# Kernel tuning notes

Hardware: AMD Instinct MI355X
Metric: run time of the kernel (lower is better)

## Reference

```python
import jax, jax.numpy as jnp
import numpy as np

N_NODES = 50000
N_EDGES = 600000
IN_F = 128
OUT_F = 128
SMALL = max(IN_F // 10, 1)  # floor(128/10) = 12
D_K = np.sqrt(SMALL).astype(np.float32)


def setup_inputs() -> dict:
    key = jax.random.key(0)
    ks = jax.random.split(key, 10)
    node_data = jax.random.normal(ks[0], (N_NODES, IN_F), dtype=jnp.float32)
    src = jax.random.randint(ks[1], (N_EDGES,), 0, N_NODES, dtype=jnp.int32)
    dst = jax.random.randint(ks[2], (N_EDGES,), 0, N_NODES, dtype=jnp.int32)
    s_q = 1.0 / np.sqrt(IN_F)
    Wq = jax.random.uniform(ks[3], (SMALL, IN_F), jnp.float32, -s_q, s_q)
    bq = jax.random.uniform(ks[4], (SMALL,), jnp.float32, -s_q, s_q)
    Wk = jax.random.uniform(ks[5], (SMALL, IN_F), jnp.float32, -s_q, s_q)
    bk = jax.random.uniform(ks[6], (SMALL,), jnp.float32, -s_q, s_q)
    W1 = jax.random.uniform(ks[7], (OUT_F, IN_F), jnp.float32, -s_q, s_q)
    W2 = jax.random.uniform(ks[8], (OUT_F, IN_F), jnp.float32, -s_q, s_q)
    b2 = jax.random.uniform(ks[9], (OUT_F,), jnp.float32, -s_q, s_q)
    return {"node_data": node_data, "src": src, "dst": dst,
            "Wq": Wq, "bq": bq, "Wk": Wk, "bk": bk,
            "W1": W1, "W2": W2, "b2": b2}


def reference(node_data, src, dst, Wq, bq, Wk, bk, W1, W2, b2):
    N = node_data.shape[0]
    # dgl.add_self_loop: append (i, i) for every node -> each dst has >= 1 edge
    loops = jnp.arange(N, dtype=src.dtype)
    s = jnp.concatenate([src, loops])
    d = jnp.concatenate([dst, loops])

    # query = Tanh(Linear), key = Linear  (shapes [N, SMALL])
    q = jnp.tanh(node_data @ Wq.T + bq)
    k = node_data @ Wk.T + bk

    # per-edge score: sum(query[src] * key[dst]) / sqrt(small)
    scores = jnp.sum(q[s] * k[d], axis=1) / D_K  # [E]

    # softmax over incoming edges of each dst node (segment softmax)
    seg_max = jax.ops.segment_max(scores, d, num_segments=N)
    w = jnp.exp(scores - seg_max[d])
    seg_sum = jax.ops.segment_sum(w, d, num_segments=N)
    w = w / seg_sum[d]  # [E]

    # weighted scatter-aggregate of src node inputs -> [N, IN_F]
    att = jax.ops.segment_sum(w[:, None] * node_data[s], d, num_segments=N)

    # DeepSetLayer: layer1(node_data) + layer2(node attention)
    x = node_data @ W1.T + (att @ W2.T + b2)
    # per-row L2 ('fro' over dim=1) normalization, then ReLU
    x = x / jnp.linalg.norm(x, axis=1, keepdims=True)
    return jax.nn.relu(x)
```

## Files before the change

kernel.cpp:

```cpp
#include <hip/hip_runtime.h>
#include <hip/hip_bf16.h>
#include <math.h>
#include <stdint.h>


#define IN_F 128
#define SMALL 12
#define QK_PAD 16

#define SCAN_ITEMS 8
#define SCAN_CHUNK 2048

typedef __attribute__((ext_vector_type(8))) short short8;
typedef __attribute__((ext_vector_type(4))) float f32x4;

__device__ __forceinline__ unsigned short f2bf(float f) {
    union { float f; unsigned u; } v; v.f = f;
    unsigned r = v.u + 0x7fff + ((v.u >> 16) & 1);
    return (unsigned short)(r >> 16);
}

__device__ __forceinline__ float2 bf2x2(unsigned v) {
    union { unsigned u; float f; } a, b;
    a.u = v << 16;
    b.u = v & 0xffff0000u;
    return make_float2(a.f, b.f);
}

__device__ __forceinline__ float dot12(const float* __restrict__ qrow,
                                       float4 k0, float4 k1, float4 k2) {
    float4 a = ((const float4*)qrow)[0];
    float4 b = ((const float4*)qrow)[1];
    float4 c = ((const float4*)qrow)[2];
    return a.x*k0.x + a.y*k0.y + a.z*k0.z + a.w*k0.w
         + b.x*k1.x + b.y*k1.y + b.z*k1.z + b.w*k1.w
         + c.x*k2.x + c.y*k2.y + c.z*k2.z + c.w*k2.w;
}

__device__ __forceinline__ short8 ld_bf8(const float* p) {
    float4 x0 = *(const float4*)p;
    float4 x1 = *(const float4*)(p + 4);
    short8 a;
    a[0] = (short)f2bf(x0.x); a[1] = (short)f2bf(x0.y);
    a[2] = (short)f2bf(x0.z); a[3] = (short)f2bf(x0.w);
    a[4] = (short)f2bf(x1.x); a[5] = (short)f2bf(x1.y);
    a[6] = (short)f2bf(x1.z); a[7] = (short)f2bf(x1.w);
    return a;
}

__global__ __launch_bounds__(256) void prep_kernel(
    const float* __restrict__ nd,
    const float* __restrict__ Wq, const float* __restrict__ bq,
    const float* __restrict__ Wk, const float* __restrict__ bk,
    const int* __restrict__ dst,
    const float* __restrict__ W1, const float* __restrict__ W2,
    float* __restrict__ q, float* __restrict__ kf,
    unsigned short* __restrict__ ndb, int* __restrict__ cnt,
    unsigned short* __restrict__ rank, unsigned short* __restrict__ Wc,
    int N, int E, int NBQK, int NBCNT)
{
    int t = threadIdx.x;
    int b = blockIdx.x;

    if (b < NBQK) {
        int wv = t >> 6;
        int lane = t & 63;
        int col = lane & 15;
        int quad = lane >> 4;
        int tbase = b * 64 + wv * 16;

        int arow = tbase + col;
        int rowc = (arow < N) ? arow : (N - 1);
        const float* ap = nd + (size_t)rowc * IN_F + quad * 8;
        unsigned short* np = ndb + (size_t)arow * IN_F + quad * 8;

        const float* w0 = ((col < 12) ? (Wq + (size_t)col * IN_F)
                                      : (Wk + (size_t)(col - 12) * IN_F)) + quad * 8;
        const float* w1 = Wk + (size_t)((col < 8) ? (col + 4) : 4) * IN_F + quad * 8;
        bool hasw1 = (col < 8);

        f32x4 acc0 = (f32x4)0.f, acc1 = (f32x4)0.f;
#pragma unroll
        for (int ks = 0; ks < 4; ks++) {
            int k0 = ks * 32;
            short8 a = ld_bf8(ap + k0);
            if (arow < N) *(short8*)(np + k0) = a;
            short8 b0 = ld_bf8(w0 + k0);
            short8 b1 = hasw1 ? ld_bf8(w1 + k0) : (short8)0;
            acc0 = __builtin_amdgcn_mfma_f32_16x16x32_bf16(a, b0, acc0, 0, 0, 0);
            acc1 = __builtin_amdgcn_mfma_f32_16x16x32_bf16(a, b1, acc1, 0, 0, 0);
        }

        float bias0 = (col < 12) ? bq[col] : bk[col - 12];
        float bias1 = (col < 8) ? bk[col + 4] : 0.f;
#pragma unroll
        for (int r = 0; r < 4; r++) {
            int node = tbase + quad * 4 + r;
            if (node < N) {
                float v0 = acc0[r] + bias0;
                if (col < 12) {
                    q[(size_t)node * QK_PAD + col] = tanhf(v0);
                } else {
                    kf[(size_t)node * QK_PAD + (col - 12)] = v0;
                }
                if (hasw1)
                    kf[(size_t)node * QK_PAD + col + 4] = acc1[r] + bias1;
            }
        }
    } else if (b < NBQK + NBCNT) {
        int ET = E + N;
        int stride = NBCNT * 256;
        for (int i = (b - NBQK) * 256 + t; i < ET; i += stride) {
            int d = (i < E) ? dst[i] : (i - E);
            rank[i] = (unsigned short)atomicAdd(&cnt[d], 1);
        }
    } else {
        int idx = (b - NBQK - NBCNT) * 256 + t;
        int f = idx >> 8, k = idx & 255;
        float v = (k < 128) ? W1[f * 128 + k] : W2[f * 128 + (k - 128)];
        Wc[idx] = f2bf(v);
    }
}

__global__ __launch_bounds__(256) void scan_local_kernel(
    int* __restrict__ off, int* __restrict__ bsum, int N)
{
    __shared__ int tsum[256];
    int t = threadIdx.x;
    int base = blockIdx.x * SCAN_CHUNK + t * SCAN_ITEMS;
    int v[SCAN_ITEMS];
    int s = 0;
#pragma unroll
    for (int i = 0; i < SCAN_ITEMS; i++) {
        int idx = base + i;
        v[i] = (idx < N) ? off[idx] : 0;
        s += v[i];
    }
    tsum[t] = s;
    __syncthreads();
    for (int d = 1; d < 256; d <<= 1) {
        int x = (t >= d) ? tsum[t - d] : 0;
        __syncthreads();
        tsum[t] += x;
        __syncthreads();
    }
    int excl = (t == 0) ? 0 : tsum[t - 1];
#pragma unroll
    for (int i = 0; i < SCAN_ITEMS; i++) {
        int idx = base + i;
        if (idx < N) off[idx] = excl;
        excl += v[i];
    }
    if (t == 255) bsum[blockIdx.x] = tsum[255];
}

__global__ __launch_bounds__(256) void scan_add_kernel(
    int* __restrict__ off, const int* __restrict__ bsum, int N, int NB)
{
    __shared__ int pre2[2];
    int t = threadIdx.x;
    if (t == 0) {
        int p = 0, tot = 0;
        for (int i = 0; i < NB; i++) {
            int v = bsum[i];
            if (i < (int)blockIdx.x) p += v;
            tot += v;
        }
        pre2[0] = p; pre2[1] = tot;
    }
    __syncthreads();
    int add = pre2[0];
    if (blockIdx.x == 0 && t == 0) off[N] = pre2[1];

    int base = blockIdx.x * SCAN_CHUNK + t * SCAN_ITEMS;
#pragma unroll
    for (int i = 0; i < SCAN_ITEMS; i++) {
        int j = base + i;
        if (j < N) off[j] += add;
    }
}

__global__ __launch_bounds__(256) void scatter_kernel(
    const int* __restrict__ src, const int* __restrict__ dst,
    const int* __restrict__ off, const unsigned short* __restrict__ rank,
    unsigned short* __restrict__ esrc, int E, int N)
{
    int i = blockIdx.x * 256 + threadIdx.x;
    if (i >= E + N) return;
    int d, s;
    if (i < E) { d = dst[i]; s = src[i]; }
    else       { d = i - E; s = d; }
    esrc[off[d] + (int)rank[i]] = (unsigned short)s;
}

__global__ __launch_bounds__(256) void attn_kernel(
    const unsigned short* __restrict__ ndb, const float* __restrict__ q,
    const float* __restrict__ kf, const int* __restrict__ off,
    const unsigned short* __restrict__ esrc, float* __restrict__ att, int N)
{
    const float INVDK = 0.28867513459481287f;
    int wid = blockIdx.x * 4 + (threadIdx.x >> 6);
    if (wid >= N) return;
    int lane = threadIdx.x & 63;

    int start = off[wid];
    int deg = off[wid + 1] - start;

    const float4* kp = (const float4*)(kf + (size_t)wid * QK_PAD);
    float4 k0 = kp[0], k1 = kp[1], k2 = kp[2];

    float2 acc = make_float2(0.f, 0.f);
    float inv;

    if (deg <= 64) {
        float sc = -INFINITY;
        int si = 0;
        if (lane < deg) {
            si = (int)esrc[start + lane];
            sc = dot12(q + (size_t)si * QK_PAD, k0, k1, k2) * INVDK;
        }
        float m = sc;
#pragma unroll
        for (int o = 32; o > 0; o >>= 1) m = fmaxf(m, __shfl_xor(m, o));
        float w = (lane < deg) ? __expf(sc - m) : 0.f;
        float lsum = w;
#pragma unroll
        for (int o = 32; o > 0; o >>= 1) lsum += __shfl_xor(lsum, o);
        inv = 1.f / lsum;

        unsigned cur[16], nxt[16];
#pragma unroll
        for (int u = 0; u < 16; u++) {
            int r = __shfl(si, u);
            if (u < deg)
                cur[u] = *(const unsigned*)(ndb + (size_t)r * IN_F + lane * 2);
        }
        for (int b0 = 0; b0 < deg; b0 += 16) {
#pragma unroll
            for (int u = 0; u < 16; u++) {
                int idx = b0 + 16 + u;
                int r = __shfl(si, idx & 63);
                if (idx < deg)
                    nxt[u] = *(const unsigned*)(ndb + (size_t)r * IN_F + lane * 2);
            }
#pragma unroll
            for (int u = 0; u < 16; u++) {
                int idx = b0 + u;
                if (idx < deg) {
                    float wi = __shfl(w, idx);
                    float2 f = bf2x2(cur[u]);
                    acc.x += wi * f.x;
                    acc.y += wi * f.y;
                }
            }
#pragma unroll
            for (int u = 0; u < 16; u++) cur[u] = nxt[u];
        }
    } else {
        float m = -INFINITY;
        for (int i = lane; i < deg; i += 64) {
            int s2 = (int)esrc[start + i];
            m = fmaxf(m, dot12(q + (size_t)s2 * QK_PAD, k0, k1, k2) * INVDK);
        }
#pragma unroll
        for (int o = 32; o > 0; o >>= 1) m = fmaxf(m, __shfl_xor(m, o));
        float lsum = 0.f;
        for (int i = lane; i < deg; i += 64) {
            int s2 = (int)esrc[start + i];
            lsum += __expf(dot12(q + (size_t)s2 * QK_PAD, k0, k1, k2) * INVDK - m);
        }
#pragma unroll
        for (int o = 32; o > 0; o >>= 1) lsum += __shfl_xor(lsum, o);
        inv = 1.f / lsum;
        for (int base = 0; base < deg; base += 64) {
            int cnt2 = deg - base; if (cnt2 > 64) cnt2 = 64;
            float w = 0.f; int si = 0;
            if (lane < cnt2) {
                si = (int)esrc[start + base + lane];
                w = __expf(dot12(q + (size_t)si * QK_PAD, k0, k1, k2) * INVDK - m);
            }
            for (int i = 0; i < cnt2; i++) {
                float wi = __shfl(w, i);
                int r = __shfl(si, i);
                float2 f = bf2x2(*(const unsigned*)(ndb + (size_t)r * IN_F + lane * 2));
                acc.x += wi * f.x;
                acc.y += wi * f.y;
            }
        }
    }
    acc.x *= inv; acc.y *= inv;
    ((float2*)(att + (size_t)wid * IN_F))[lane] = acc;
}

__global__ __launch_bounds__(256) void final_kernel(
    const unsigned short* __restrict__ ndb, const float* __restrict__ nd,
    const float* __restrict__ att,
    const unsigned short* __restrict__ Wc, const float* __restrict__ b2,
    float* __restrict__ out, int N)
{
    int wv = threadIdx.x >> 6;
    int lane = threadIdx.x & 63;
    int col = lane & 15;
    int quad = lane >> 4;

    int arow = blockIdx.x * 64 + wv * 16 + col;
    int rowc = (arow < N) ? arow : (N - 1);
    const unsigned short* a0p = ndb + (size_t)rowc * IN_F + quad * 8;
    const float* a1p = ((arow < N) ? att : nd) + (size_t)rowc * IN_F + quad * 8;

    f32x4 acc[8];
#pragma unroll
    for (int i = 0; i < 8; i++) acc[i] = (f32x4)0.f;

#pragma unroll
    for (int ks = 0; ks < 8; ks++) {
        int k0 = ks * 32;
        short8 a;
        if (ks < 4) {
            a = *(const short8*)(a0p + k0);
        } else {
            a = ld_bf8(a1p + (k0 - 128));
        }
#pragma unroll
        for (int ft = 0; ft < 8; ft++) {
            int n = ft * 16 + col;
            short8 b = *(const short8*)(Wc + (size_t)n * 256 + k0 + quad * 8);
            acc[ft] = __builtin_amdgcn_mfma_f32_16x16x32_bf16(a, b, acc[ft], 0, 0, 0);
        }
    }

    float bias[8];
#pragma unroll
    for (int ft = 0; ft < 8; ft++) bias[ft] = b2[ft * 16 + col];

#pragma unroll
    for (int r = 0; r < 4; r++) {
        int node = blockIdx.x * 64 + wv * 16 + quad * 4 + r;
        float v[8];
        float ps = 0.f;
#pragma unroll
        for (int ft = 0; ft < 8; ft++) {
            v[ft] = acc[ft][r] + bias[ft];
            ps += v[ft] * v[ft];
        }
        ps += __shfl_xor(ps, 1);
        ps += __shfl_xor(ps, 2);
        ps += __shfl_xor(ps, 4);
        ps += __shfl_xor(ps, 8);
        float rn = rsqrtf(ps);
        if (node < N) {
            float* op = out + (size_t)node * 128 + col;
#pragma unroll
            for (int ft = 0; ft < 8; ft++)
                op[ft * 16] = fmaxf(v[ft] * rn, 0.f);
        }
    }
}

static inline char* align_up(char* p, size_t a) {
    return (char*)(((uintptr_t)p + (a - 1)) & ~(uintptr_t)(a - 1));
}

extern "C" void kernel_launch(void* const* d_in, const int* in_sizes, int n_in,
                              void* d_out, int out_size, void* d_ws, size_t ws_size,
                              hipStream_t stream) {
    const float* node_data = (const float*)d_in[0];
    const int*   src       = (const int*)d_in[1];
    const int*   dst       = (const int*)d_in[2];
    const float* Wq        = (const float*)d_in[3];
    const float* bq        = (const float*)d_in[4];
    const float* Wk        = (const float*)d_in[5];
    const float* bk        = (const float*)d_in[6];
    const float* W1        = (const float*)d_in[7];
    const float* W2        = (const float*)d_in[8];
    const float* b2        = (const float*)d_in[9];
    float* out = (float*)d_out;

    int N = in_sizes[0] / IN_F;
    int E = in_sizes[1];
    int ET = E + N;
    int NB = (N + SCAN_CHUNK - 1) / SCAN_CHUNK;
    int NBQK = (N + 63) / 64;
    int NBCNT = 512;
    int NBCVT = 128;

    char* w = (char*)d_ws;
    float* q  = (float*)w;  w += (size_t)N * QK_PAD * sizeof(float);
    float* kf = (float*)w;  w += (size_t)N * QK_PAD * sizeof(float);
    w = align_up(w, 256);
    unsigned short* ndb = (unsigned short*)w;  w += (size_t)N * IN_F * sizeof(unsigned short);
    w = align_up(w, 256);
    unsigned short* Wc = (unsigned short*)w;  w += 128 * 256 * sizeof(unsigned short);
    int* off    = (int*)w;  w += (size_t)(N + 1) * sizeof(int);
    int* bsum   = (int*)w;  w += 256 * sizeof(int);
    unsigned short* rank = (unsigned short*)w;  w += (size_t)ET * sizeof(unsigned short);
    w = align_up(w, 256);
    unsigned short* esrc = (unsigned short*)w;  w += (size_t)ET * sizeof(unsigned short);
    float* att = out;

    hipMemsetAsync(off, 0, (size_t)(N + 1) * sizeof(int), stream);

    prep_kernel<<<NBQK + NBCNT + NBCVT, 256, 0, stream>>>(
        node_data, Wq, bq, Wk, bk, dst, W1, W2,
        q, kf, ndb, off, rank, Wc, N, E, NBQK, NBCNT);
    scan_local_kernel<<<NB, 256, 0, stream>>>(off, bsum, N);
    scan_add_kernel<<<NB, 256, 0, stream>>>(off, bsum, N, NB);
    scatter_kernel<<<(ET + 255) / 256, 256, 0, stream>>>(src, dst, off, rank, esrc, E, N);
    attn_kernel<<<(N + 3) / 4, 256, 0, stream>>>(ndb, q, kf, off, esrc, att, N);
    final_kernel<<<(N + 63) / 64, 256, 0, stream>>>(ndb, node_data, att, Wc, b2, out, N);
}
```

Measured before the change: 226.6 us.

## Fuse all stages into one persistent cooperative kernel with grid syncs

Replaces the memset plus six separate kernel launches with a single cooperative persistent kernel that loops over work with grid-stride loops and separates the stages with grid.sync(). It also simplifies the attention gather loop from a 16-deep double-buffered prefetch to a 4-way unrolled loop. The intent is to remove launch overhead and inter-kernel gaps. In exchange it limits parallelism to one resident grid of at most 1024 blocks, pays for six grid-wide barriers, and hides less gather latency.

```diff
diff --git a/kernel.cpp b/kernel.cpp
--- a/kernel.cpp
+++ b/kernel.cpp
@@ -1,13 +1,15 @@
 #include <hip/hip_runtime.h>
+#include <hip/hip_cooperative_groups.h>
 #include <hip/hip_bf16.h>
 #include <math.h>
 #include <stdint.h>
 
+namespace cg = cooperative_groups;
+
 
 #define IN_F 128
 #define SMALL 12
 #define QK_PAD 16
-
 #define SCAN_ITEMS 8
 #define SCAN_CHUNK 2048
 
@@ -28,13 +30,13 @@
 }
 
 __device__ __forceinline__ float dot12(const float* __restrict__ qrow,
-                                       float4 k0, float4 k1, float4 k2) {
+                                       float4 c0, float4 c1, float4 c2) {
     float4 a = ((const float4*)qrow)[0];
     float4 b = ((const float4*)qrow)[1];
     float4 c = ((const float4*)qrow)[2];
-    return a.x*k0.x + a.y*k0.y + a.z*k0.z + a.w*k0.w
-         + b.x*k1.x + b.y*k1.y + b.z*k1.z + b.w*k1.w
-         + c.x*k2.x + c.y*k2.y + c.z*k2.z + c.w*k2.w;
+    return a.x*c0.x + a.y*c0.y + a.z*c0.z + a.w*c0.w
+         + b.x*c1.x + b.y*c1.y + b.z*c1.z + b.w*c1.w
+         + c.x*c2.x + c.y*c2.y + c.z*c2.z + c.w*c2.w;
 }
 
 __device__ __forceinline__ short8 ld_bf8(const float* p) {
@@ -48,27 +50,40 @@
     return a;
 }
 
-__global__ __launch_bounds__(256) void prep_kernel(
-    const float* __restrict__ nd,
+__global__ __launch_bounds__(256, 4) void mega_kernel(
+    const float* __restrict__ nd, const int* __restrict__ src,
+    const int* __restrict__ dst,
     const float* __restrict__ Wq, const float* __restrict__ bq,
     const float* __restrict__ Wk, const float* __restrict__ bk,
-    const int* __restrict__ dst,
     const float* __restrict__ W1, const float* __restrict__ W2,
+    const float* __restrict__ b2,
     float* __restrict__ q, float* __restrict__ kf,
-    unsigned short* __restrict__ ndb, int* __restrict__ cnt,
-    unsigned short* __restrict__ rank, unsigned short* __restrict__ Wc,
-    int N, int E, int NBQK, int NBCNT)
+    unsigned short* __restrict__ ndb, unsigned short* __restrict__ Wc,
+    int* __restrict__ off, int* __restrict__ bsum,
+    unsigned short* __restrict__ rank, unsigned short* __restrict__ esrc,
+    float* __restrict__ out, int N, int E)
 {
+    cg::grid_group grid = cg::this_grid();
+    __shared__ int tsum[256];
+    __shared__ int pre2[2];
+
     int t = threadIdx.x;
     int b = blockIdx.x;
-
-    if (b < NBQK) {
-        int wv = t >> 6;
-        int lane = t & 63;
-        int col = lane & 15;
-        int quad = lane >> 4;
-        int tbase = b * 64 + wv * 16;
-
+    int NBLK = gridDim.x;
+    int gsz = NBLK * 256;
+    int gid = b * 256 + t;
+    int ET = E + N;
+    int wv = t >> 6;
+    int lane = t & 63;
+    int col = lane & 15;
+    int quad = lane >> 4;
+    int NT = (N + 63) >> 6;
+
+    for (int i = gid; i <= N; i += gsz) off[i] = 0;
+    grid.sync();
+
+    for (int tb = b; tb < NT; tb += NBLK) {
+        int tbase = tb * 64 + wv * 16;
         int arow = tbase + col;
         int rowc = (arow < N) ? arow : (N - 1);
         const float* ap = nd + (size_t)rowc * IN_F + quad * 8;
@@ -85,12 +100,11 @@
             int k0 = ks * 32;
             short8 a = ld_bf8(ap + k0);
             if (arow < N) *(short8*)(np + k0) = a;
-            short8 b0 = ld_bf8(w0 + k0);
-            short8 b1 = hasw1 ? ld_bf8(w1 + k0) : (short8)0;
-            acc0 = __builtin_amdgcn_mfma_f32_16x16x32_bf16(a, b0, acc0, 0, 0, 0);
-            acc1 = __builtin_amdgcn_mfma_f32_16x16x32_bf16(a, b1, acc1, 0, 0, 0);
-        }
-
+            short8 bb0 = ld_bf8(w0 + k0);
+            short8 bb1 = hasw1 ? ld_bf8(w1 + k0) : (short8)0;
+            acc0 = __builtin_amdgcn_mfma_f32_16x16x32_bf16(a, bb0, acc0, 0, 0, 0);
+            acc1 = __builtin_amdgcn_mfma_f32_16x16x32_bf16(a, bb1, acc1, 0, 0, 0);
+        }
         float bias0 = (col < 12) ? bq[col] : bk[col - 12];
         float bias1 = (col < 8) ? bk[col + 4] : 0.f;
 #pragma unroll
@@ -98,261 +112,224 @@
             int node = tbase + quad * 4 + r;
             if (node < N) {
                 float v0 = acc0[r] + bias0;
-                if (col < 12) {
-                    q[(size_t)node * QK_PAD + col] = tanhf(v0);
-                } else {
-                    kf[(size_t)node * QK_PAD + (col - 12)] = v0;
-                }
-                if (hasw1)
-                    kf[(size_t)node * QK_PAD + col + 4] = acc1[r] + bias1;
-            }
-        }
-    } else if (b < NBQK + NBCNT) {
-        int ET = E + N;
-        int stride = NBCNT * 256;
-        for (int i = (b - NBQK) * 256 + t; i < ET; i += stride) {
-            int d = (i < E) ? dst[i] : (i - E);
-            rank[i] = (unsigned short)atomicAdd(&cnt[d], 1);
-        }
-    } else {
-        int idx = (b - NBQK - NBCNT) * 256 + t;
-        int f = idx >> 8, k = idx & 255;
+                if (col < 12) q[(size_t)node * QK_PAD + col] = tanhf(v0);
+                else          kf[(size_t)node * QK_PAD + (col - 12)] = v0;
+                if (hasw1)    kf[(size_t)node * QK_PAD + col + 4] = acc1[r] + bias1;
+            }
+        }
+    }
+    for (int i = gid; i < ET; i += gsz) {
+        int d = (i < E) ? dst[i] : (i - E);
+        rank[i] = (unsigned short)atomicAdd(&off[d], 1);
+    }
+    for (int i = gid; i < 128 * 256; i += gsz) {
+        int f = i >> 8, k = i & 255;
         float v = (k < 128) ? W1[f * 128 + k] : W2[f * 128 + (k - 128)];
-        Wc[idx] = f2bf(v);
-    }
-}
-
-__global__ __launch_bounds__(256) void scan_local_kernel(
-    int* __restrict__ off, int* __restrict__ bsum, int N)
-{
-    __shared__ int tsum[256];
-    int t = threadIdx.x;
-    int base = blockIdx.x * SCAN_CHUNK + t * SCAN_ITEMS;
-    int v[SCAN_ITEMS];
-    int s = 0;
-#pragma unroll
-    for (int i = 0; i < SCAN_ITEMS; i++) {
-        int idx = base + i;
-        v[i] = (idx < N) ? off[idx] : 0;
-        s += v[i];
-    }
-    tsum[t] = s;
-    __syncthreads();
-    for (int d = 1; d < 256; d <<= 1) {
-        int x = (t >= d) ? tsum[t - d] : 0;
+        Wc[i] = f2bf(v);
+    }
+    grid.sync();
+
+    int NBS = (N + SCAN_CHUNK - 1) / SCAN_CHUNK;
+    if (b < NBS) {
+        int base = b * SCAN_CHUNK + t * SCAN_ITEMS;
+        int v[SCAN_ITEMS];
+        int s = 0;
+#pragma unroll
+        for (int i = 0; i < SCAN_ITEMS; i++) {
+            int idx = base + i;
+            v[i] = (idx < N) ? off[idx] : 0;
+            s += v[i];
+        }
+        tsum[t] = s;
         __syncthreads();
-        tsum[t] += x;
+        for (int d = 1; d < 256; d <<= 1) {
+            int x = (t >= d) ? tsum[t - d] : 0;
+            __syncthreads();
+            tsum[t] += x;
+            __syncthreads();
+        }
+        int excl = (t == 0) ? 0 : tsum[t - 1];
+#pragma unroll
+        for (int i = 0; i < SCAN_ITEMS; i++) {
+            int idx = base + i;
+            if (idx < N) off[idx] = excl;
+            excl += v[i];
+        }
+        if (t == 255) bsum[b] = tsum[255];
+    }
+    grid.sync();
+
+    if (b < NBS) {
+        if (t == 0) {
+            int p = 0, tot = 0;
+            for (int i = 0; i < NBS; i++) {
+                int v = bsum[i];
+                if (i < b) p += v;
+                tot += v;
+            }
+            pre2[0] = p; pre2[1] = tot;
+        }
         __syncthreads();
-    }
-    int excl = (t == 0) ? 0 : tsum[t - 1];
-#pragma unroll
-    for (int i = 0; i < SCAN_ITEMS; i++) {
-        int idx = base + i;
-        if (idx < N) off[idx] = excl;
-        excl += v[i];
-    }
-    if (t == 255) bsum[blockIdx.x] = tsum[255];
-}
-
-__global__ __launch_bounds__(256) void scan_add_kernel(
-    int* __restrict__ off, const int* __restrict__ bsum, int N, int NB)
-{
-    __shared__ int pre2[2];
-    int t = threadIdx.x;
-    if (t == 0) {
-        int p = 0, tot = 0;
-        for (int i = 0; i < NB; i++) {
-            int v = bsum[i];
-            if (i < (int)blockIdx.x) p += v;
-            tot += v;
-        }
-        pre2[0] = p; pre2[1] = tot;
-    }
-    __syncthreads();
-    int add = pre2[0];
-    if (blockIdx.x == 0 && t == 0) off[N] = pre2[1];
-
-    int base = blockIdx.x * SCAN_CHUNK + t * SCAN_ITEMS;
-#pragma unroll
-    for (int i = 0; i < SCAN_ITEMS; i++) {
-        int j = base + i;
-        if (j < N) off[j] += add;
-    }
-}
-
-__global__ __launch_bounds__(256) void scatter_kernel(
-    const int* __restrict__ src, const int* __restrict__ dst,
-    const int* __restrict__ off, const unsigned short* __restrict__ rank,
-    unsigned short* __restrict__ esrc, int E, int N)
-{
-    int i = blockIdx.x * 256 + threadIdx.x;
-    if (i >= E + N) return;
-    int d, s;
-    if (i < E) { d = dst[i]; s = src[i]; }
-    else       { d = i - E; s = d; }
-    esrc[off[d] + (int)rank[i]] = (unsigned short)s;
-}
-
-__global__ __launch_bounds__(256) void attn_kernel(
-    const unsigned short* __restrict__ ndb, const float* __restrict__ q,
-    const float* __restrict__ kf, const int* __restrict__ off,
-    const unsigned short* __restrict__ esrc, float* __restrict__ att, int N)
-{
-    const float INVDK = 0.28867513459481287f;
-    int wid = blockIdx.x * 4 + (threadIdx.x >> 6);
-    if (wid >= N) return;
-    int lane = threadIdx.x & 63;
-
-    int start = off[wid];
-    int deg = off[wid + 1] - start;
-
-    const float4* kp = (const float4*)(kf + (size_t)wid * QK_PAD);
-    float4 k0 = kp[0], k1 = kp[1], k2 = kp[2];
-
-    float2 acc = make_float2(0.f, 0.f);
-    float inv;
-
-    if (deg <= 64) {
-        float sc = -INFINITY;
-        int si = 0;
-        if (lane < deg) {
-            si = (int)esrc[start + lane];
-            sc = dot12(q + (size_t)si * QK_PAD, k0, k1, k2) * INVDK;
-        }
-        float m = sc;
-#pragma unroll
-        for (int o = 32; o > 0; o >>= 1) m = fmaxf(m, __shfl_xor(m, o));
-        float w = (lane < deg) ? __expf(sc - m) : 0.f;
-        float lsum = w;
-#pragma unroll
-        for (int o = 32; o > 0; o >>= 1) lsum += __shfl_xor(lsum, o);
-        inv = 1.f / lsum;
-
-        unsigned cur[16], nxt[16];
-#pragma unroll
-        for (int u = 0; u < 16; u++) {
-            int r = __shfl(si, u);
-            if (u < deg)
-                cur[u] = *(const unsigned*)(ndb + (size_t)r * IN_F + lane * 2);
-        }
-        for (int b0 = 0; b0 < deg; b0 += 16) {
-#pragma unroll
-            for (int u = 0; u < 16; u++) {
-                int idx = b0 + 16 + u;
-                int r = __shfl(si, idx & 63);
-                if (idx < deg)
-                    nxt[u] = *(const unsigned*)(ndb + (size_t)r * IN_F + lane * 2);
-            }
-#pragma unroll
-            for (int u = 0; u < 16; u++) {
-                int idx = b0 + u;
-                if (idx < deg) {
-                    float wi = __shfl(w, idx);
-                    float2 f = bf2x2(cur[u]);
+        int add = pre2[0];
+        if (b == 0 && t == 0) off[N] = pre2[1];
+        int base = b * SCAN_CHUNK + t * SCAN_ITEMS;
+#pragma unroll
+        for (int i = 0; i < SCAN_ITEMS; i++) {
+            int j = base + i;
+            if (j < N) off[j] += add;
+        }
+    }
+    grid.sync();
+
+    for (int i = gid; i < ET; i += gsz) {
+        int d, s;
+        if (i < E) { d = dst[i]; s = src[i]; }
+        else       { d = i - E; s = d; }
+        esrc[off[d] + (int)rank[i]] = (unsigned short)s;
+    }
+    grid.sync();
+
+    {
+        const float INVDK = 0.28867513459481287f;
+        float* att = out;
+        for (int wid = b * 4 + wv; wid < N; wid += NBLK * 4) {
+            int start = off[wid];
+            int deg = off[wid + 1] - start;
+
+            const float4* kp = (const float4*)(kf + (size_t)wid * QK_PAD);
+            float4 c0 = kp[0], c1 = kp[1], c2 = kp[2];
+
+            float2 acc = make_float2(0.f, 0.f);
+            float inv;
+
+            if (deg <= 64) {
+                float sc = -INFINITY;
+                int si = 0;
+                if (lane < deg) {
+                    si = (int)esrc[start + lane];
+                    sc = dot12(q + (size_t)si * QK_PAD, c0, c1, c2) * INVDK;
+                }
+                float m = sc;
+#pragma unroll
+                for (int o = 32; o > 0; o >>= 1) m = fmaxf(m, __shfl_xor(m, o));
+                float w = (lane < deg) ? __expf(sc - m) : 0.f;
+                float lsum = w;
+#pragma unroll
+                for (int o = 32; o > 0; o >>= 1) lsum += __shfl_xor(lsum, o);
+                inv = 1.f / lsum;
+
+                int i = 0;
+                for (; i + 4 <= deg; i += 4) {
+                    float w0 = __shfl(w, i);     int r0 = __shfl(si, i);
+                    float w1 = __shfl(w, i + 1); int r1 = __shfl(si, i + 1);
+                    float w2 = __shfl(w, i + 2); int r2 = __shfl(si, i + 2);
+                    float w3 = __shfl(w, i + 3); int r3 = __shfl(si, i + 3);
+                    unsigned v0 = *(const unsigned*)(ndb + (size_t)r0 * IN_F + lane * 2);
+                    unsigned v1 = *(const unsigned*)(ndb + (size_t)r1 * IN_F + lane * 2);
+                    unsigned v2 = *(const unsigned*)(ndb + (size_t)r2 * IN_F + lane * 2);
+                    unsigned v3 = *(const unsigned*)(ndb + (size_t)r3 * IN_F + lane * 2);
+                    float2 f0 = bf2x2(v0), f1 = bf2x2(v1), f2 = bf2x2(v2), f3 = bf2x2(v3);
+                    acc.x += w0 * f0.x + w1 * f1.x + w2 * f2.x + w3 * f3.x;
+                    acc.y += w0 * f0.y + w1 * f1.y + w2 * f2.y + w3 * f3.y;
+                }
+                for (; i < deg; i++) {
+                    float wi = __shfl(w, i);
+                    int r = __shfl(si, i);
+                    float2 f = bf2x2(*(const unsigned*)(ndb + (size_t)r * IN_F + lane * 2));
                     acc.x += wi * f.x;
                     acc.y += wi * f.y;
                 }
-            }
-#pragma unroll
-            for (int u = 0; u < 16; u++) cur[u] = nxt[u];
-        }
-    } else {
-        float m = -INFINITY;
-        for (int i = lane; i < deg; i += 64) {
-            int s2 = (int)esrc[start + i];
-            m = fmaxf(m, dot12(q + (size_t)s2 * QK_PAD, k0, k1, k2) * INVDK);
-        }
-#pragma unroll
-        for (int o = 32; o > 0; o >>= 1) m = fmaxf(m, __shfl_xor(m, o));
-        float lsum = 0.f;
-        for (int i = lane; i < deg; i += 64) {
-            int s2 = (int)esrc[start + i];
-            lsum += __expf(dot12(q + (size_t)s2 * QK_PAD, k0, k1, k2) * INVDK - m);
-        }
-#pragma unroll
-        for (int o = 32; o > 0; o >>= 1) lsum += __shfl_xor(lsum, o);
-        inv = 1.f / lsum;
-        for (int base = 0; base < deg; base += 64) {
-            int cnt2 = deg - base; if (cnt2 > 64) cnt2 = 64;
-            float w = 0.f; int si = 0;
-            if (lane < cnt2) {
-                si = (int)esrc[start + base + lane];
-                w = __expf(dot12(q + (size_t)si * QK_PAD, k0, k1, k2) * INVDK - m);
-            }
-            for (int i = 0; i < cnt2; i++) {
-                float wi = __shfl(w, i);
-                int r = __shfl(si, i);
-                float2 f = bf2x2(*(const unsigned*)(ndb + (size_t)r * IN_F + lane * 2));
-                acc.x += wi * f.x;
-                acc.y += wi * f.y;
-            }
-        }
-    }
-    acc.x *= inv; acc.y *= inv;
-    ((float2*)(att + (size_t)wid * IN_F))[lane] = acc;
-}
-
-__global__ __launch_bounds__(256) void final_kernel(
-    const unsigned short* __restrict__ ndb, const float* __restrict__ nd,
-    const float* __restrict__ att,
-    const unsigned short* __restrict__ Wc, const float* __restrict__ b2,
-    float* __restrict__ out, int N)
-{
-    int wv = threadIdx.x >> 6;
-    int lane = threadIdx.x & 63;
-    int col = lane & 15;
-    int quad = lane >> 4;
-
-    int arow = blockIdx.x * 64 + wv * 16 + col;
-    int rowc = (arow < N) ? arow : (N - 1);
-    const unsigned short* a0p = ndb + (size_t)rowc * IN_F + quad * 8;
-    const float* a1p = ((arow < N) ? att : nd) + (size_t)rowc * IN_F + quad * 8;
-
-    f32x4 acc[8];
-#pragma unroll
-    for (int i = 0; i < 8; i++) acc[i] = (f32x4)0.f;
-
-#pragma unroll
-    for (int ks = 0; ks < 8; ks++) {
-        int k0 = ks * 32;
-        short8 a;
-        if (ks < 4) {
-            a = *(const short8*)(a0p + k0);
-        } else {
-            a = ld_bf8(a1p + (k0 - 128));
-        }
-#pragma unroll
-        for (int ft = 0; ft < 8; ft++) {
-            int n = ft * 16 + col;
-            short8 b = *(const short8*)(Wc + (size_t)n * 256 + k0 + quad * 8);
-            acc[ft] = __builtin_amdgcn_mfma_f32_16x16x32_bf16(a, b, acc[ft], 0, 0, 0);
-        }
-    }
-
-    float bias[8];
-#pragma unroll
-    for (int ft = 0; ft < 8; ft++) bias[ft] = b2[ft * 16 + col];
-
-#pragma unroll
-    for (int r = 0; r < 4; r++) {
-        int node = blockIdx.x * 64 + wv * 16 + quad * 4 + r;
-        float v[8];
-        float ps = 0.f;
-#pragma unroll
-        for (int ft = 0; ft < 8; ft++) {
-            v[ft] = acc[ft][r] + bias[ft];
-            ps += v[ft] * v[ft];
-        }
-        ps += __shfl_xor(ps, 1);
-        ps += __shfl_xor(ps, 2);
-        ps += __shfl_xor(ps, 4);
-        ps += __shfl_xor(ps, 8);
-        float rn = rsqrtf(ps);
-        if (node < N) {
-            float* op = out + (size_t)node * 128 + col;
-#pragma unroll
-            for (int ft = 0; ft < 8; ft++)
-                op[ft * 16] = fmaxf(v[ft] * rn, 0.f);
+            } else {
+                float m = -INFINITY;
+                for (int i = lane; i < deg; i += 64) {
+                    int s2 = (int)esrc[start + i];
+                    m = fmaxf(m, dot12(q + (size_t)s2 * QK_PAD, c0, c1, c2) * INVDK);
+                }
+#pragma unroll
+                for (int o = 32; o > 0; o >>= 1) m = fmaxf(m, __shfl_xor(m, o));
+                float lsum = 0.f;
+                for (int i = lane; i < deg; i += 64) {
+                    int s2 = (int)esrc[start + i];
+                    lsum += __expf(dot12(q + (size_t)s2 * QK_PAD, c0, c1, c2) * INVDK - m);
+                }
+#pragma unroll
+                for (int o = 32; o > 0; o >>= 1) lsum += __shfl_xor(lsum, o);
+                inv = 1.f / lsum;
+                for (int base2 = 0; base2 < deg; base2 += 64) {
+                    int cnt2 = deg - base2; if (cnt2 > 64) cnt2 = 64;
+                    float w = 0.f; int si = 0;
+                    if (lane < cnt2) {
+                        si = (int)esrc[start + base2 + lane];
+                        w = __expf(dot12(q + (size_t)si * QK_PAD, c0, c1, c2) * INVDK - m);
+                    }
+                    for (int i = 0; i < cnt2; i++) {
+                        float wi = __shfl(w, i);
+                        int r = __shfl(si, i);
+                        float2 f = bf2x2(*(const unsigned*)(ndb + (size_t)r * IN_F + lane * 2));
+                        acc.x += wi * f.x;
+                        acc.y += wi * f.y;
+                    }
+                }
+            }
+            acc.x *= inv; acc.y *= inv;
+            ((float2*)(att + (size_t)wid * IN_F))[lane] = acc;
+        }
+    }
+    grid.sync();
+
+    {
+        const float* att = out;
+        for (int tb = b; tb < NT; tb += NBLK) {
+            int nbase = tb * 64;
+            int arow = nbase + wv * 16 + col;
+            int rowc = (arow < N) ? arow : (N - 1);
+            const unsigned short* a0p = ndb + (size_t)rowc * IN_F + quad * 8;
+            const float* a1p = ((arow < N) ? att : nd) + (size_t)rowc * IN_F + quad * 8;
+
+            f32x4 acc[8];
+#pragma unroll
+            for (int i = 0; i < 8; i++) acc[i] = (f32x4)0.f;
+
+#pragma unroll
+            for (int ks = 0; ks < 8; ks++) {
+                int k0 = ks * 32;
+                short8 a;
+                if (ks < 4) a = *(const short8*)(a0p + k0);
+                else        a = ld_bf8(a1p + (k0 - 128));
+#pragma unroll
+                for (int ft = 0; ft < 8; ft++) {
+                    int n = ft * 16 + col;
+                    short8 bb = *(const short8*)(Wc + (size_t)n * 256 + k0 + quad * 8);
+                    acc[ft] = __builtin_amdgcn_mfma_f32_16x16x32_bf16(a, bb, acc[ft], 0, 0, 0);
+                }
+            }
+
+            float bias[8];
+#pragma unroll
+            for (int ft = 0; ft < 8; ft++) bias[ft] = b2[ft * 16 + col];
+
+#pragma unroll
+            for (int r = 0; r < 4; r++) {
+                int node = nbase + wv * 16 + quad * 4 + r;
+                float v[8];
+                float ps = 0.f;
+#pragma unroll
+                for (int ft = 0; ft < 8; ft++) {
+                    v[ft] = acc[ft][r] + bias[ft];
+                    ps += v[ft] * v[ft];
+                }
+                ps += __shfl_xor(ps, 1);
+                ps += __shfl_xor(ps, 2);
+                ps += __shfl_xor(ps, 4);
+                ps += __shfl_xor(ps, 8);
+                float rn = rsqrtf(ps);
+                if (node < N) {
+                    float* op = out + (size_t)node * 128 + col;
+#pragma unroll
+                    for (int ft = 0; ft < 8; ft++)
+                        op[ft * 16] = fmaxf(v[ft] * rn, 0.f);
+                }
+            }
         }
     }
 }
@@ -379,10 +356,6 @@
     int N = in_sizes[0] / IN_F;
     int E = in_sizes[1];
     int ET = E + N;
-    int NB = (N + SCAN_CHUNK - 1) / SCAN_CHUNK;
-    int NBQK = (N + 63) / 64;
-    int NBCNT = 512;
-    int NBCVT = 128;
 
     char* w = (char*)d_ws;
     float* q  = (float*)w;  w += (size_t)N * QK_PAD * sizeof(float);
@@ -391,21 +364,26 @@
     unsigned short* ndb = (unsigned short*)w;  w += (size_t)N * IN_F * sizeof(unsigned short);
     w = align_up(w, 256);
     unsigned short* Wc = (unsigned short*)w;  w += 128 * 256 * sizeof(unsigned short);
-    int* off    = (int*)w;  w += (size_t)(N + 1) * sizeof(int);
-    int* bsum   = (int*)w;  w += 256 * sizeof(int);
+    int* off  = (int*)w;  w += (size_t)(N + 1) * sizeof(int);
+    int* bsum = (int*)w;  w += 1024 * sizeof(int);
     unsigned short* rank = (unsigned short*)w;  w += (size_t)ET * sizeof(unsigned short);
     w = align_up(w, 256);
     unsigned short* esrc = (unsigned short*)w;  w += (size_t)ET * sizeof(unsigned short);
-    float* att = out;
-
-    hipMemsetAsync(off, 0, (size_t)(N + 1) * sizeof(int), stream);
-
-    prep_kernel<<<NBQK + NBCNT + NBCVT, 256, 0, stream>>>(
-        node_data, Wq, bq, Wk, bk, dst, W1, W2,
-        q, kf, ndb, off, rank, Wc, N, E, NBQK, NBCNT);
-    scan_local_kernel<<<NB, 256, 0, stream>>>(off, bsum, N);
-    scan_add_kernel<<<NB, 256, 0, stream>>>(off, bsum, N, NB);
-    scatter_kernel<<<(ET + 255) / 256, 256, 0, stream>>>(src, dst, off, rank, esrc, E, N);
-    attn_kernel<<<(N + 3) / 4, 256, 0, stream>>>(ndb, q, kf, off, esrc, att, N);
-    final_kernel<<<(N + 63) / 64, 256, 0, stream>>>(ndb, node_data, att, Wc, b2, out, N);
-}
+
+    int occ = 0;
+    hipOccupancyMaxActiveBlocksPerMultiprocessor(&occ, mega_kernel, 256, 0);
+    if (occ < 1) occ = 1;
+    long long grid_ll = (long long)occ * 256;
+    int grid = (grid_ll > 1024) ? 1024 : (int)grid_ll;
+
+    void* args[] = {
+        (void*)&node_data, (void*)&src, (void*)&dst,
+        (void*)&Wq, (void*)&bq, (void*)&Wk, (void*)&bk,
+        (void*)&W1, (void*)&W2, (void*)&b2,
+        (void*)&q, (void*)&kf, (void*)&ndb, (void*)&Wc,
+        (void*)&off, (void*)&bsum, (void*)&rank, (void*)&esrc,
+        (void*)&out, (void*)&N, (void*)&E
+    };
+    hipLaunchCooperativeKernel((const void*)mega_kernel, dim3(grid), dim3(256),
+                               args, 0, stream);
+}
```

After: 628.8 us. +177.5%, slower.

## Fuse attention aggregation into final GEMM kernel via shared-memory bf16 tile

Applied to the files above, without the earlier changes.

Merges the attention aggregation kernel and the final DeepSet GEMM/normalize kernel into one. Each block aggregates 64 destination nodes, with each wave looping over 16 nodes, and stores the results as bf16 in LDS. It then runs the MFMA GEMM straight from LDS, which removes the fp32 att round trip through global memory and one launch. The aggregation loop also changes from a 16-deep register prefetch to a 4-way unrolled gather. The trade-off is less parallelism, since there are 4x fewer waves per node and each wave processes 16 nodes serially, so gather latency may be hidden less well.

```diff
diff --git a/kernel.cpp b/kernel.cpp
--- a/kernel.cpp
+++ b/kernel.cpp
@@ -7,9 +7,9 @@
 #define IN_F 128
 #define SMALL 12
 #define QK_PAD 16
-
 #define SCAN_ITEMS 8
 #define SCAN_CHUNK 2048
+#define ALD 136
 
 typedef __attribute__((ext_vector_type(8))) short short8;
 typedef __attribute__((ext_vector_type(4))) float f32x4;
@@ -28,13 +28,13 @@
 }
 
 __device__ __forceinline__ float dot12(const float* __restrict__ qrow,
-                                       float4 k0, float4 k1, float4 k2) {
+                                       float4 c0, float4 c1, float4 c2) {
     float4 a = ((const float4*)qrow)[0];
     float4 b = ((const float4*)qrow)[1];
     float4 c = ((const float4*)qrow)[2];
-    return a.x*k0.x + a.y*k0.y + a.z*k0.z + a.w*k0.w
-         + b.x*k1.x + b.y*k1.y + b.z*k1.z + b.w*k1.w
-         + c.x*k2.x + c.y*k2.y + c.z*k2.z + c.w*k2.w;
+    return a.x*c0.x + a.y*c0.y + a.z*c0.z + a.w*c0.w
+         + b.x*c1.x + b.y*c1.y + b.z*c1.z + b.w*c1.w
+         + c.x*c2.x + c.y*c2.y + c.z*c2.z + c.w*c2.w;
 }
 
 __device__ __forceinline__ short8 ld_bf8(const float* p) {
@@ -85,12 +85,11 @@
             int k0 = ks * 32;
             short8 a = ld_bf8(ap + k0);
             if (arow < N) *(short8*)(np + k0) = a;
-            short8 b0 = ld_bf8(w0 + k0);
-            short8 b1 = hasw1 ? ld_bf8(w1 + k0) : (short8)0;
-            acc0 = __builtin_amdgcn_mfma_f32_16x16x32_bf16(a, b0, acc0, 0, 0, 0);
-            acc1 = __builtin_amdgcn_mfma_f32_16x16x32_bf16(a, b1, acc1, 0, 0, 0);
-        }
-
+            short8 bb0 = ld_bf8(w0 + k0);
+            short8 bb1 = hasw1 ? ld_bf8(w1 + k0) : (short8)0;
+            acc0 = __builtin_amdgcn_mfma_f32_16x16x32_bf16(a, bb0, acc0, 0, 0, 0);
+            acc1 = __builtin_amdgcn_mfma_f32_16x16x32_bf16(a, bb1, acc1, 0, 0, 0);
+        }
         float bias0 = (col < 12) ? bq[col] : bk[col - 12];
         float bias1 = (col < 8) ? bk[col + 4] : 0.f;
 #pragma unroll
@@ -98,13 +97,9 @@
             int node = tbase + quad * 4 + r;
             if (node < N) {
                 float v0 = acc0[r] + bias0;
-                if (col < 12) {
-                    q[(size_t)node * QK_PAD + col] = tanhf(v0);
-                } else {
-                    kf[(size_t)node * QK_PAD + (col - 12)] = v0;
-                }
-                if (hasw1)
-                    kf[(size_t)node * QK_PAD + col + 4] = acc1[r] + bias1;
+                if (col < 12) q[(size_t)node * QK_PAD + col] = tanhf(v0);
+                else          kf[(size_t)node * QK_PAD + (col - 12)] = v0;
+                if (hasw1)    kf[(size_t)node * QK_PAD + col + 4] = acc1[r] + bias1;
             }
         }
     } else if (b < NBQK + NBCNT) {
@@ -193,120 +188,115 @@
     esrc[off[d] + (int)rank[i]] = (unsigned short)s;
 }
 
-__global__ __launch_bounds__(256) void attn_kernel(
+__global__ __launch_bounds__(256) void attn_final_kernel(
     const unsigned short* __restrict__ ndb, const float* __restrict__ q,
     const float* __restrict__ kf, const int* __restrict__ off,
-    const unsigned short* __restrict__ esrc, float* __restrict__ att, int N)
-{
+    const unsigned short* __restrict__ esrc,
+    const unsigned short* __restrict__ Wc, const float* __restrict__ b2,
+    float* __restrict__ out, int N)
+{
+    __shared__ unsigned short att_lds[64][ALD];
+
     const float INVDK = 0.28867513459481287f;
-    int wid = blockIdx.x * 4 + (threadIdx.x >> 6);
-    if (wid >= N) return;
-    int lane = threadIdx.x & 63;
-
-    int start = off[wid];
-    int deg = off[wid + 1] - start;
-
-    const float4* kp = (const float4*)(kf + (size_t)wid * QK_PAD);
-    float4 k0 = kp[0], k1 = kp[1], k2 = kp[2];
-
-    float2 acc = make_float2(0.f, 0.f);
-    float inv;
-
-    if (deg <= 64) {
-        float sc = -INFINITY;
-        int si = 0;
-        if (lane < deg) {
-            si = (int)esrc[start + lane];
-            sc = dot12(q + (size_t)si * QK_PAD, k0, k1, k2) * INVDK;
-        }
-        float m = sc;
-#pragma unroll
-        for (int o = 32; o > 0; o >>= 1) m = fmaxf(m, __shfl_xor(m, o));
-        float w = (lane < deg) ? __expf(sc - m) : 0.f;
-        float lsum = w;
-#pragma unroll
-        for (int o = 32; o > 0; o >>= 1) lsum += __shfl_xor(lsum, o);
-        inv = 1.f / lsum;
-
-        unsigned cur[16], nxt[16];
-#pragma unroll
-        for (int u = 0; u < 16; u++) {
-            int r = __shfl(si, u);
-            if (u < deg)
-                cur[u] = *(const unsigned*)(ndb + (size_t)r * IN_F + lane * 2);
-        }
-        for (int b0 = 0; b0 < deg; b0 += 16) {
-#pragma unroll
-            for (int u = 0; u < 16; u++) {
-                int idx = b0 + 16 + u;
-                int r = __shfl(si, idx & 63);
-                if (idx < deg)
-                    nxt[u] = *(const unsigned*)(ndb + (size_t)r * IN_F + lane * 2);
-            }
-#pragma unroll
-            for (int u = 0; u < 16; u++) {
-                int idx = b0 + u;
-                if (idx < deg) {
-                    float wi = __shfl(w, idx);
-                    float2 f = bf2x2(cur[u]);
-                    acc.x += wi * f.x;
-                    acc.y += wi * f.y;
-                }
-            }
-#pragma unroll
-            for (int u = 0; u < 16; u++) cur[u] = nxt[u];
-        }
-    } else {
-        float m = -INFINITY;
-        for (int i = lane; i < deg; i += 64) {
-            int s2 = (int)esrc[start + i];
-            m = fmaxf(m, dot12(q + (size_t)s2 * QK_PAD, k0, k1, k2) * INVDK);
-        }
-#pragma unroll
-        for (int o = 32; o > 0; o >>= 1) m = fmaxf(m, __shfl_xor(m, o));
-        float lsum = 0.f;
-        for (int i = lane; i < deg; i += 64) {
-            int s2 = (int)esrc[start + i];
-            lsum += __expf(dot12(q + (size_t)s2 * QK_PAD, k0, k1, k2) * INVDK - m);
-        }
-#pragma unroll
-        for (int o = 32; o > 0; o >>= 1) lsum += __shfl_xor(lsum, o);
-        inv = 1.f / lsum;
-        for (int base = 0; base < deg; base += 64) {
-            int cnt2 = deg - base; if (cnt2 > 64) cnt2 = 64;
-            float w = 0.f; int si = 0;
-            if (lane < cnt2) {
-                si = (int)esrc[start + base + lane];
-                w = __expf(dot12(q + (size_t)si * QK_PAD, k0, k1, k2) * INVDK - m);
-            }
-            for (int i = 0; i < cnt2; i++) {
+    int t = threadIdx.x;
+    int wv = t >> 6;
+    int lane = t & 63;
+    int col = lane & 15;
+    int quad = lane >> 4;
+    int nbase = blockIdx.x * 64;
+
+    for (int it = 0; it < 16; it++) {
+        int wid = nbase + wv * 16 + it;
+        if (wid >= N) break;
+
+        int start = off[wid];
+        int deg = off[wid + 1] - start;
+
+        const float4* kp = (const float4*)(kf + (size_t)wid * QK_PAD);
+        float4 c0 = kp[0], c1 = kp[1], c2 = kp[2];
+
+        float2 acc = make_float2(0.f, 0.f);
+        float inv;
+
+        if (deg <= 64) {
+            float sc = -INFINITY;
+            int si = 0;
+            if (lane < deg) {
+                si = (int)esrc[start + lane];
+                sc = dot12(q + (size_t)si * QK_PAD, c0, c1, c2) * INVDK;
+            }
+            float m = sc;
+#pragma unroll
+            for (int o = 32; o > 0; o >>= 1) m = fmaxf(m, __shfl_xor(m, o));
+            float w = (lane < deg) ? __expf(sc - m) : 0.f;
+            float lsum = w;
+#pragma unroll
+            for (int o = 32; o > 0; o >>= 1) lsum += __shfl_xor(lsum, o);
+            inv = 1.f / lsum;
+
+            int i = 0;
+            for (; i + 4 <= deg; i += 4) {
+                float w0 = __shfl(w, i);     int r0 = __shfl(si, i);
+                float w1 = __shfl(w, i + 1); int r1 = __shfl(si, i + 1);
+                float w2 = __shfl(w, i + 2); int r2 = __shfl(si, i + 2);
+                float w3 = __shfl(w, i + 3); int r3 = __shfl(si, i + 3);
+                unsigned v0 = *(const unsigned*)(ndb + (size_t)r0 * IN_F + lane * 2);
+                unsigned v1 = *(const unsigned*)(ndb + (size_t)r1 * IN_F + lane * 2);
+                unsigned v2 = *(const unsigned*)(ndb + (size_t)r2 * IN_F + lane * 2);
+                unsigned v3 = *(const unsigned*)(ndb + (size_t)r3 * IN_F + lane * 2);
+                float2 f0 = bf2x2(v0), f1 = bf2x2(v1), f2 = bf2x2(v2), f3 = bf2x2(v3);
+                acc.x += w0 * f0.x + w1 * f1.x + w2 * f2.x + w3 * f3.x;
+                acc.y += w0 * f0.y + w1 * f1.y + w2 * f2.y + w3 * f3.y;
+            }
+            for (; i < deg; i++) {
                 float wi = __shfl(w, i);
                 int r = __shfl(si, i);
                 float2 f = bf2x2(*(const unsigned*)(ndb + (size_t)r * IN_F + lane * 2));
                 acc.x += wi * f.x;
                 acc.y += wi * f.y;
             }
-        }
-    }
-    acc.x *= inv; acc.y *= inv;
-    ((float2*)(att + (size_t)wid * IN_F))[lane] = acc;
-}
-
-__global__ __launch_bounds__(256) void final_kernel(
-    const unsigned short* __restrict__ ndb, const float* __restrict__ nd,
-    const float* __restrict__ att,
-    const unsigned short* __restrict__ Wc, const float* __restrict__ b2,
-    float* __restrict__ out, int N)
-{
-    int wv = threadIdx.x >> 6;
-    int lane = threadIdx.x & 63;
-    int col = lane & 15;
-    int quad = lane >> 4;
-
-    int arow = blockIdx.x * 64 + wv * 16 + col;
+        } else {
+            float m = -INFINITY;
+            for (int i = lane; i < deg; i += 64) {
+                int s2 = (int)esrc[start + i];
+                m = fmaxf(m, dot12(q + (size_t)s2 * QK_PAD, c0, c1, c2) * INVDK);
+            }
+#pragma unroll
+            for (int o = 32; o > 0; o >>= 1) m = fmaxf(m, __shfl_xor(m, o));
+            float lsum = 0.f;
+            for (int i = lane; i < deg; i += 64) {
+                int s2 = (int)esrc[start + i];
+                lsum += __expf(dot12(q + (size_t)s2 * QK_PAD, c0, c1, c2) * INVDK - m);
+            }
+#pragma unroll
+            for (int o = 32; o > 0; o >>= 1) lsum += __shfl_xor(lsum, o);
+            inv = 1.f / lsum;
+            for (int base2 = 0; base2 < deg; base2 += 64) {
+                int cnt2 = deg - base2; if (cnt2 > 64) cnt2 = 64;
+                float w = 0.f; int si = 0;
+                if (lane < cnt2) {
+                    si = (int)esrc[start + base2 + lane];
+                    w = __expf(dot12(q + (size_t)si * QK_PAD, c0, c1, c2) * INVDK - m);
+                }
+                for (int i = 0; i < cnt2; i++) {
+                    float wi = __shfl(w, i);
+                    int r = __shfl(si, i);
+                    float2 f = bf2x2(*(const unsigned*)(ndb + (size_t)r * IN_F + lane * 2));
+                    acc.x += wi * f.x;
+                    acc.y += wi * f.y;
+                }
+            }
+        }
+        acc.x *= inv; acc.y *= inv;
+        unsigned pak = (unsigned)f2bf(acc.x) | ((unsigned)f2bf(acc.y) << 16);
+        *(unsigned*)&att_lds[wv * 16 + it][lane * 2] = pak;
+    }
+    __syncthreads();
+
+    int arow = nbase + wv * 16 + col;
     int rowc = (arow < N) ? arow : (N - 1);
     const unsigned short* a0p = ndb + (size_t)rowc * IN_F + quad * 8;
-    const float* a1p = ((arow < N) ? att : nd) + (size_t)rowc * IN_F + quad * 8;
+    const unsigned short* alp = &att_lds[wv * 16 + col][quad * 8];
 
     f32x4 acc[8];
 #pragma unroll
@@ -316,16 +306,13 @@
     for (int ks = 0; ks < 8; ks++) {
         int k0 = ks * 32;
         short8 a;
-        if (ks < 4) {
-            a = *(const short8*)(a0p + k0);
-        } else {
-            a = ld_bf8(a1p + (k0 - 128));
-        }
+        if (ks < 4) a = *(const short8*)(a0p + k0);
+        else        a = *(const short8*)(alp + (k0 - 128));
 #pragma unroll
         for (int ft = 0; ft < 8; ft++) {
             int n = ft * 16 + col;
-            short8 b = *(const short8*)(Wc + (size_t)n * 256 + k0 + quad * 8);
-            acc[ft] = __builtin_amdgcn_mfma_f32_16x16x32_bf16(a, b, acc[ft], 0, 0, 0);
+            short8 bb = *(const short8*)(Wc + (size_t)n * 256 + k0 + quad * 8);
+            acc[ft] = __builtin_amdgcn_mfma_f32_16x16x32_bf16(a, bb, acc[ft], 0, 0, 0);
         }
     }
 
@@ -335,7 +322,7 @@
 
 #pragma unroll
     for (int r = 0; r < 4; r++) {
-        int node = blockIdx.x * 64 + wv * 16 + quad * 4 + r;
+        int node = nbase + wv * 16 + quad * 4 + r;
         float v[8];
         float ps = 0.f;
 #pragma unroll
@@ -383,6 +370,7 @@
     int NBQK = (N + 63) / 64;
     int NBCNT = 512;
     int NBCVT = 128;
+    int NT = (N + 63) / 64;
 
     char* w = (char*)d_ws;
     float* q  = (float*)w;  w += (size_t)N * QK_PAD * sizeof(float);
@@ -391,12 +379,11 @@
     unsigned short* ndb = (unsigned short*)w;  w += (size_t)N * IN_F * sizeof(unsigned short);
     w = align_up(w, 256);
     unsigned short* Wc = (unsigned short*)w;  w += 128 * 256 * sizeof(unsigned short);
-    int* off    = (int*)w;  w += (size_t)(N + 1) * sizeof(int);
-    int* bsum   = (int*)w;  w += 256 * sizeof(int);
+    int* off  = (int*)w;  w += (size_t)(N + 1) * sizeof(int);
+    int* bsum = (int*)w;  w += 256 * sizeof(int);
     unsigned short* rank = (unsigned short*)w;  w += (size_t)ET * sizeof(unsigned short);
     w = align_up(w, 256);
     unsigned short* esrc = (unsigned short*)w;  w += (size_t)ET * sizeof(unsigned short);
-    float* att = out;
 
     hipMemsetAsync(off, 0, (size_t)(N + 1) * sizeof(int), stream);
 
@@ -406,6 +393,5 @@
     scan_local_kernel<<<NB, 256, 0, stream>>>(off, bsum, N);
     scan_add_kernel<<<NB, 256, 0, stream>>>(off, bsum, N, NB);
     scatter_kernel<<<(ET + 255) / 256, 256, 0, stream>>>(src, dst, off, rank, esrc, E, N);
-    attn_kernel<<<(N + 3) / 4, 256, 0, stream>>>(ndb, q, kf, off, esrc, att, N);
-    final_kernel<<<(N + 63) / 64, 256, 0, stream>>>(ndb, node_data, att, Wc, b2, out, N);
-}
+    attn_final_kernel<<<NT, 256, 0, stream>>>(ndb, q, kf, off, esrc, Wc, b2, out, N);
+}
```

Measured after the change: 231.8 us. 1.02x slower.
